# Optimization experiments

Hardware: AMD Instinct MI355X
Metric: run time of the kernel (lower is better)

The kernel has to match this reference:

```python
import jax, jax.numpy as jnp
import numpy as np

B, T, D, H = 4, 1024, 512, 8
DH = D // H
MLP = 4 * D
EPS = 1e-6


def _clinear(xr, xi, Wr, Wi, br, bi):
    # Naive complex Linear = two real nn.Linear layers (each adds its own bias):
    # re = Lr(xr) - Li(xi), im = Lr(xi) + Li(xr)
    re = xr @ Wr.T - xi @ Wi.T + (br - bi)
    im = xi @ Wr.T + xr @ Wi.T + (br + bi)
    return re, im


def _cln(xr, xi):
    # NaiveComplexLayerNorm: real LayerNorm (no affine) on re and im separately
    def ln(v):
        m = jnp.mean(v, -1, keepdims=True)
        va = jnp.var(v, -1, keepdims=True)
        return (v - m) * jax.lax.rsqrt(va + EPS)
    return ln(xr), ln(xi)


def _modulate(xr, xi, shr, shi, scr, sci):
    # complex x * (1 + scale) + shift, scale/shift are [B,D] broadcast over seq
    a, b = (1.0 + scr)[:, None, :], sci[:, None, :]
    return xr * a - xi * b + shr[:, None, :], xr * b + xi * a + shi[:, None, :]


def _gate(gr, gi, xr, xi):
    a, b = gr[:, None, :], gi[:, None, :]
    return xr * a - xi * b, xr * b + xi * a


def _heads(x):  # [B,T,D] -> [B,H,T,DH]
    return x.reshape(B, T, H, DH).transpose(0, 2, 1, 3)


def reference(x_re, x_im, c_re, c_im,
              ada_Wr, ada_Wi, ada_br, ada_bi,
              q_Wr, q_Wi, q_br, q_bi,
              k_Wr, k_Wi, k_br, k_bi,
              v_Wr, v_Wi, v_br, v_bi,
              o_Wr, o_Wi, o_br, o_bi,
              f1_Wr, f1_Wi, f1_br, f1_bi,
              f2_Wr, f2_Wi, f2_br, f2_bi):
    # adaLN_modulation: complex SiLU -> complex Linear -> 6 chunks along dim 1
    sr, si = jax.nn.silu(c_re), jax.nn.silu(c_im)
    mr, mi = _clinear(sr, si, ada_Wr, ada_Wi, ada_br, ada_bi)
    sh_ar, sc_ar, g_ar, sh_mr, sc_mr, g_mr = jnp.split(mr, 6, axis=1)
    sh_ai, sc_ai, g_ai, sh_mi, sc_mi, g_mi = jnp.split(mi, 6, axis=1)

    nr, ni = _cln(x_re, x_im)
    hr, hi = _modulate(nr, ni, sh_ar, sh_ai, sc_ar, sc_ai)

    qr, qi = _clinear(hr, hi, q_Wr, q_Wi, q_br, q_bi)
    kr, ki = _clinear(hr, hi, k_Wr, k_Wi, k_br, k_bi)
    vr, vi = _clinear(hr, hi, v_Wr, v_Wi, v_br, v_bi)
    qr, qi, kr, ki, vr, vi = map(_heads, (qr, qi, kr, ki, vr, vi))

    scale = 1.0 / jnp.sqrt(jnp.float32(DH))
    # complex scores q @ k^T (no conjugation, matching plain complex matmul)
    s_re = (jnp.einsum('bhqd,bhkd->bhqk', qr, kr) - jnp.einsum('bhqd,bhkd->bhqk', qi, ki)) * scale
    s_im = (jnp.einsum('bhqd,bhkd->bhqk', qr, ki) + jnp.einsum('bhqd,bhkd->bhqk', qi, kr)) * scale
    # naive complex softmax: real softmax applied to re/im independently
    a_re = jax.nn.softmax(s_re, axis=-1)
    a_im = jax.nn.softmax(s_im, axis=-1)
    o_r = jnp.einsum('bhqk,bhkd->bhqd', a_re, vr) - jnp.einsum('bhqk,bhkd->bhqd', a_im, vi)
    o_i = jnp.einsum('bhqk,bhkd->bhqd', a_re, vi) + jnp.einsum('bhqk,bhkd->bhqd', a_im, vr)
    o_r = o_r.transpose(0, 2, 1, 3).reshape(B, T, D)
    o_i = o_i.transpose(0, 2, 1, 3).reshape(B, T, D)
    o_r, o_i = _clinear(o_r, o_i, o_Wr, o_Wi, o_br, o_bi)

    gr, gi = _gate(g_ar, g_ai, o_r, o_i)
    x_re, x_im = x_re + gr, x_im + gi

    # ---- MLP branch
    nr, ni = _cln(x_re, x_im)
    hr, hi = _modulate(nr, ni, sh_mr, sh_mi, sc_mr, sc_mi)
    hr, hi = _clinear(hr, hi, f1_Wr, f1_Wi, f1_br, f1_bi)
    hr = jax.nn.gelu(hr, approximate=True)  # ComplexGELU(tanh) per component
    hi = jax.nn.gelu(hi, approximate=True)
    hr, hi = _clinear(hr, hi, f2_Wr, f2_Wi, f2_br, f2_bi)
    gr, gi = _gate(g_mr, g_mi, hr, hi)
    return jnp.stack([x_re + gr, x_im + gi])  # [2,B,T,D] = (real, imag)


def setup_inputs() -> dict:
    key = jax.random.key(0)
    ks = iter(jax.random.split(key, 48))

    def rn(shape, s=1.0):
        return jax.random.normal(next(ks), shape, dtype=jnp.float32) * s

    inp = {'x_re': rn((B, T, D)), 'x_im': rn((B, T, D)),
           'c_re': rn((B, D)), 'c_im': rn((B, D))}

    def lin(name, din, dout):
        inp[name + '_Wr'] = rn((dout, din), 0.02)
        inp[name + '_Wi'] = rn((dout, din), 0.02)
        inp[name + '_br'] = rn((dout,), 0.02)
        inp[name + '_bi'] = rn((dout,), 0.02)

    lin('ada', D, 6 * D)
    for n in ('q', 'k', 'v', 'o'):
        lin(n, D, D)
    lin('f1', D, MLP)
    lin('f2', MLP, D)
    return inp
```

## Files before the change

kernel.cpp:

```cpp
#include <hip/hip_runtime.h>


typedef unsigned short u16;
typedef __attribute__((ext_vector_type(8))) __bf16 bf16x8;
typedef __attribute__((ext_vector_type(8))) u16    u16x8;
typedef __attribute__((ext_vector_type(4))) u16    u16x4;
typedef __attribute__((ext_vector_type(4))) float  f32x4;

#define MFMA16(a, b, c) __builtin_amdgcn_mfma_f32_16x16x32_bf16(a, b, c, 0, 0, 0)

static constexpr int Bd = 4, Td = 1024, Dd = 512, Hd = 8, DHd = 64, MLPd = 2048;

__device__ __forceinline__ u16 f2bf(float x) {
  unsigned int u = __builtin_bit_cast(unsigned int, x);
  u += 0x7fffu + ((u >> 16) & 1u);
  return (u16)(u >> 16);
}
__device__ __forceinline__ bf16x8 ldsfrag(const u16* p) {
  return __builtin_bit_cast(bf16x8, *(const u16x8*)p);
}
__device__ __forceinline__ bf16x8 negbf(bf16x8 v) {
  u16x8 u = __builtin_bit_cast(u16x8, v);
  u ^= (u16)0x8000;
  return __builtin_bit_cast(bf16x8, u);
}
__device__ __forceinline__ float gelu_tanh(float x) {
  float t = tanhf(0.7978845608028654f * (x + 0.044715f * x * x * x));
  return 0.5f * x * (1.f + t);
}

struct CJobs {
  const float* src[12];
  u16* dst[12];
  int blk_start[13];
};
__global__ __launch_bounds__(256) void convert_kernel(CJobs J) {
  const int blk = blockIdx.x;
  int jj = 0;
  while (jj < 11 && blk >= J.blk_start[jj + 1]) ++jj;
  const int idx = (blk - J.blk_start[jj]) * 256 + threadIdx.x;
  const float4 v = ((const float4*)J.src[jj])[idx];
  u16x4 o;
  o[0] = f2bf(v.x); o[1] = f2bf(v.y); o[2] = f2bf(v.z); o[3] = f2bf(v.w);
  *(u16x4*)(J.dst[jj] + (size_t)idx * 4) = o;
}

__global__ __launch_bounds__(256) void ada_kernel(
    const float* __restrict__ c_re, const float* __restrict__ c_im,
    const float* __restrict__ Wr, const float* __restrict__ Wi,
    const float* __restrict__ br, const float* __restrict__ bi,
    float* __restrict__ m_r, float* __restrict__ m_i) {
  __shared__ __align__(16) float sr[512], si[512];
  const int b = blockIdx.x / 12, nb = blockIdx.x % 12;
  const int tid = threadIdx.x;
  for (int i = tid; i < 512; i += 256) {
    const float xr = c_re[b * 512 + i], xi = c_im[b * 512 + i];
    sr[i] = xr / (1.f + __expf(-xr));
    si[i] = xi / (1.f + __expf(-xi));
  }
  __syncthreads();
  const int n = nb * 256 + tid;
  const float4* wr4 = (const float4*)(Wr + (size_t)n * 512);
  const float4* wi4 = (const float4*)(Wi + (size_t)n * 512);
  const float4* sr4 = (const float4*)sr;
  const float4* si4 = (const float4*)si;
  float ar = 0.f, ai = 0.f;
  for (int k = 0; k < 128; ++k) {
    const float4 a_ = sr4[k], b_ = si4[k], u = wr4[k], v = wi4[k];
    ar += a_.x * u.x - b_.x * v.x + a_.y * u.y - b_.y * v.y +
          a_.z * u.z - b_.z * v.z + a_.w * u.w - b_.w * v.w;
    ai += b_.x * u.x + a_.x * v.x + b_.y * u.y + a_.y * v.y +
          b_.z * u.z + a_.z * v.z + b_.w * u.w + a_.w * v.w;
  }
  m_r[(size_t)b * 3072 + n] = ar + br[n] - bi[n];
  m_i[(size_t)b * 3072 + n] = ai + br[n] + bi[n];
}

__global__ __launch_bounds__(256) void ln_mod_kernel(
    const float* __restrict__ xr, const float* __restrict__ xi,
    const float* __restrict__ mv_r, const float* __restrict__ mv_i,
    int off_sh, int off_sc,
    u16* __restrict__ hr, u16* __restrict__ hi) {
  const int row = blockIdx.x;
  const int b = row >> 10;
  const int tid = threadIdx.x;
  const float* xrp = xr + (size_t)row * 512;
  const float* xip = xi + (size_t)row * 512;
  const float r0 = xrp[tid], r1 = xrp[tid + 256];
  const float i0 = xip[tid], i1 = xip[tid + 256];
  float s0 = r0 + r1, s1 = r0 * r0 + r1 * r1;
  float s2 = i0 + i1, s3 = i0 * i0 + i1 * i1;
  #pragma unroll
  for (int o = 32; o > 0; o >>= 1) {
    s0 += __shfl_down(s0, o); s1 += __shfl_down(s1, o);
    s2 += __shfl_down(s2, o); s3 += __shfl_down(s3, o);
  }
  __shared__ float red[4][4];
  if ((tid & 63) == 0) {
    const int wv = tid >> 6;
    red[wv][0] = s0; red[wv][1] = s1; red[wv][2] = s2; red[wv][3] = s3;
  }
  __syncthreads();
  s0 = red[0][0] + red[1][0] + red[2][0] + red[3][0];
  s1 = red[0][1] + red[1][1] + red[2][1] + red[3][1];
  s2 = red[0][2] + red[1][2] + red[2][2] + red[3][2];
  s3 = red[0][3] + red[1][3] + red[2][3] + red[3][3];
  const float mr = s0 * (1.f / 512.f), mi = s2 * (1.f / 512.f);
  const float vr = s1 * (1.f / 512.f) - mr * mr;
  const float vi = s3 * (1.f / 512.f) - mi * mi;
  const float rr = rsqrtf(vr + 1e-6f), ri = rsqrtf(vi + 1e-6f);
  const float* shr = mv_r + (size_t)b * 3072 + off_sh;
  const float* shi = mv_i + (size_t)b * 3072 + off_sh;
  const float* scr = mv_r + (size_t)b * 3072 + off_sc;
  const float* sci = mv_i + (size_t)b * 3072 + off_sc;
  #pragma unroll
  for (int jj = 0; jj < 2; ++jj) {
    const int n = tid + jj * 256;
    const float nr = ((jj ? r1 : r0) - mr) * rr;
    const float ni = ((jj ? i1 : i0) - mi) * ri;
    const float a = 1.f + scr[n], bb = sci[n];
    hr[(size_t)row * 512 + n] = f2bf(nr * a - ni * bb + shr[n]);
    hi[(size_t)row * 512 + n] = f2bf(nr * bb + ni * a + shi[n]);
  }
}

template <int EPI>
__global__ __launch_bounds__(256) void cgemm_kernel(
    const u16* __restrict__ Ar, const u16* __restrict__ Ai,
    const u16* __restrict__ W0r, const u16* __restrict__ W0i,
    const float* __restrict__ b0r, const float* __restrict__ b0i,
    const u16* __restrict__ W1r, const u16* __restrict__ W1i,
    const float* __restrict__ b1r, const float* __restrict__ b1i,
    const u16* __restrict__ W2r, const u16* __restrict__ W2i,
    const float* __restrict__ b2r, const float* __restrict__ b2i,
    int K, int ntiles_per_seg, int out_ld,
    u16* __restrict__ o0r, u16* __restrict__ o0i,
    u16* __restrict__ o1r, u16* __restrict__ o1i,
    u16* __restrict__ o2r, u16* __restrict__ o2i,
    const float* __restrict__ resid_r, const float* __restrict__ resid_i,
    const float* __restrict__ gate_r, const float* __restrict__ gate_i,
    float* __restrict__ ofr, float* __restrict__ ofi) {
  const int seg = blockIdx.y / ntiles_per_seg;
  const int n0 = (blockIdx.y % ntiles_per_seg) * 64;
  const int m0 = blockIdx.x * 64;
  const u16* Wr = (seg == 0) ? W0r : (seg == 1) ? W1r : W2r;
  const u16* Wi = (seg == 0) ? W0i : (seg == 1) ? W1i : W2i;
  const float* br = (seg == 0) ? b0r : (seg == 1) ? b1r : b2r;
  const float* bi = (seg == 0) ? b0i : (seg == 1) ? b1i : b2i;
  u16* obr = (seg == 0) ? o0r : (seg == 1) ? o1r : o2r;
  u16* obi = (seg == 0) ? o0i : (seg == 1) ? o1i : o2i;

  __shared__ __align__(16) u16 sA[2][64 * 72];
  __shared__ __align__(16) u16 sB[2][64 * 72];

  const int tid = threadIdx.x;
  const int w = tid >> 6, lane = tid & 63;
  const int wm = w >> 1, wn = w & 1;
  const int q4 = lane >> 4, c = lane & 15;

  const f32x4 z = {0.f, 0.f, 0.f, 0.f};
  f32x4 accR[2][2], accI[2][2];
  for (int a = 0; a < 2; ++a)
    for (int b2 = 0; b2 < 2; ++b2) { accR[a][b2] = z; accI[a][b2] = z; }

  for (int kt = 0; kt < K; kt += 64) {
    for (int idx = tid; idx < 512; idx += 256) {
      const int row = idx >> 3, cg = idx & 7;
      const int lo = row * 72 + cg * 8;
      *(u16x8*)&sA[0][lo] = *(const u16x8*)(Ar + (size_t)(m0 + row) * K + kt + cg * 8);
      *(u16x8*)&sA[1][lo] = *(const u16x8*)(Ai + (size_t)(m0 + row) * K + kt + cg * 8);
      *(u16x8*)&sB[0][lo] = *(const u16x8*)(Wr + (size_t)(n0 + row) * K + kt + cg * 8);
      *(u16x8*)&sB[1][lo] = *(const u16x8*)(Wi + (size_t)(n0 + row) * K + kt + cg * 8);
    }
    __syncthreads();
    #pragma unroll
    for (int kc = 0; kc < 2; ++kc) {
      bf16x8 a_r[2], a_i[2], a_n[2];
      #pragma unroll
      for (int mi = 0; mi < 2; ++mi) {
        const int off = (wm * 32 + mi * 16 + c) * 72 + kc * 32 + q4 * 8;
        a_r[mi] = ldsfrag(&sA[0][off]);
        a_i[mi] = ldsfrag(&sA[1][off]);
        a_n[mi] = negbf(a_i[mi]);
      }
      #pragma unroll
      for (int ni = 0; ni < 2; ++ni) {
        const int off = (wn * 32 + ni * 16 + c) * 72 + kc * 32 + q4 * 8;
        const bf16x8 b_r = ldsfrag(&sB[0][off]);
        const bf16x8 b_i = ldsfrag(&sB[1][off]);
        #pragma unroll
        for (int mi = 0; mi < 2; ++mi) {
          accR[mi][ni] = MFMA16(a_r[mi], b_r, accR[mi][ni]);
          accR[mi][ni] = MFMA16(a_n[mi], b_i, accR[mi][ni]);
          accI[mi][ni] = MFMA16(a_i[mi], b_r, accI[mi][ni]);
          accI[mi][ni] = MFMA16(a_r[mi], b_i, accI[mi][ni]);
        }
      }
    }
    __syncthreads();
  }

  const float scale = (EPI == 0 && seg == 0) ? 0.125f : 1.f;
  #pragma unroll
  for (int mi = 0; mi < 2; ++mi)
    #pragma unroll
    for (int ni = 0; ni < 2; ++ni) {
      const int n = n0 + wn * 32 + ni * 16 + c;
      const float biasr = br[n] - bi[n];
      const float biasi = br[n] + bi[n];
      #pragma unroll
      for (int r = 0; r < 4; ++r) {
        const int m = m0 + wm * 32 + mi * 16 + q4 * 4 + r;
        const float ore = accR[mi][ni][r] + biasr;
        const float oim = accI[mi][ni][r] + biasi;
        if (EPI == 0) {
          obr[(size_t)m * out_ld + n] = f2bf(ore * scale);
          obi[(size_t)m * out_ld + n] = f2bf(oim * scale);
        } else if (EPI == 2) {
          obr[(size_t)m * out_ld + n] = f2bf(gelu_tanh(ore));
          obi[(size_t)m * out_ld + n] = f2bf(gelu_tanh(oim));
        } else {
          const int bb = m >> 10;
          const float gr = gate_r[(size_t)bb * 3072 + n];
          const float gi = gate_i[(size_t)bb * 3072 + n];
          const size_t o = (size_t)m * 512 + n;
          ofr[o] = resid_r[o] + ore * gr - oim * gi;
          ofi[o] = resid_i[o] + ore * gi + oim * gr;
        }
      }
    }
}

__global__ __launch_bounds__(256) void attn_kernel(
    const u16* __restrict__ Qr, const u16* __restrict__ Qi,
    const u16* __restrict__ Kr, const u16* __restrict__ Ki,
    const u16* __restrict__ Vr, const u16* __restrict__ Vi,
    u16* __restrict__ Or, u16* __restrict__ Oi) {
  __shared__ __align__(16) u16 sQ[2][64 * 72];
  __shared__ __align__(16) u16 sK[2][64 * 72];
  __shared__ __align__(16) u16 sV[2][64 * 72];

  const int tid = threadIdx.x;
  const int w = tid >> 6, lane = tid & 63;
  const int q4 = lane >> 4, c = lane & 15;
  const int bh = blockIdx.y, b = bh >> 3, h = bh & 7;
  const int t0 = blockIdx.x * 64;
  const size_t base = (size_t)b * Td * Dd + h * DHd;

  for (int idx = tid; idx < 512; idx += 256) {
    const int row = idx >> 3, cg = idx & 7;
    const size_t g = base + (size_t)(t0 + row) * Dd + cg * 8;
    const int lo = row * 72 + cg * 8;
    *(u16x8*)&sQ[0][lo] = *(const u16x8*)(Qr + g);
    *(u16x8*)&sQ[1][lo] = *(const u16x8*)(Qi + g);
  }
  __syncthreads();
  bf16x8 aQr[2], aQi[2], aQn[2];
  #pragma unroll
  for (int kc = 0; kc < 2; ++kc) {
    const int off = (w * 16 + c) * 72 + kc * 32 + q4 * 8;
    aQr[kc] = ldsfrag(&sQ[0][off]);
    aQi[kc] = ldsfrag(&sQ[1][off]);
    aQn[kc] = negbf(aQi[kc]);
  }

  float mst[2][4], lst[2][4];
  #pragma unroll
  for (int p = 0; p < 2; ++p)
    for (int r = 0; r < 4; ++r) { mst[p][r] = -1e30f; lst[p][r] = 0.f; }
  const f32x4 z = {0.f, 0.f, 0.f, 0.f};
  f32x4 U1[4], U2[4], U3[4], U4[4];
  for (int i = 0; i < 4; ++i) { U1[i] = z; U2[i] = z; U3[i] = z; U4[i] = z; }

  for (int kt = 0; kt < 16; ++kt) {
    for (int idx = tid; idx < 512; idx += 256) {
      const int row = idx >> 3, cg = idx & 7;
      const size_t g = base + (size_t)(kt * 64 + row) * Dd + cg * 8;
      const int lo = row * 72 + cg * 8;
      *(u16x8*)&sK[0][lo] = *(const u16x8*)(Kr + g);
      *(u16x8*)&sK[1][lo] = *(const u16x8*)(Ki + g);
      const u16x8 vvr = *(const u16x8*)(Vr + g);
      const u16x8 vvi = *(const u16x8*)(Vi + g);
      #pragma unroll
      for (int j = 0; j < 8; ++j) {
        sV[0][(cg * 8 + j) * 72 + row] = vvr[j];
        sV[1][(cg * 8 + j) * 72 + row] = vvi[j];
      }
    }
    __syncthreads();

    f32x4 S[2][4];
    #pragma unroll
    for (int nb = 0; nb < 4; ++nb) {
      f32x4 tr = z, ti = z;
      #pragma unroll
      for (int kc = 0; kc < 2; ++kc) {
        const int off = (nb * 16 + c) * 72 + kc * 32 + q4 * 8;
        const bf16x8 bKr = ldsfrag(&sK[0][off]);
        const bf16x8 bKi = ldsfrag(&sK[1][off]);
        tr = MFMA16(aQr[kc], bKr, tr);
        tr = MFMA16(aQn[kc], bKi, tr);
        ti = MFMA16(aQi[kc], bKr, ti);
        ti = MFMA16(aQr[kc], bKi, ti);
      }
      S[0][nb] = tr; S[1][nb] = ti;
    }
    __syncthreads();

    float alpha[2][4];
    #pragma unroll
    for (int p = 0; p < 2; ++p) {
      float rs[4];
      #pragma unroll
      for (int r = 0; r < 4; ++r) {
        float tm = fmaxf(fmaxf(S[p][0][r], S[p][1][r]), fmaxf(S[p][2][r], S[p][3][r]));
        #pragma unroll
        for (int o = 1; o < 16; o <<= 1) tm = fmaxf(tm, __shfl_xor(tm, o));
        const float mn = fmaxf(mst[p][r], tm);
        alpha[p][r] = __expf(mst[p][r] - mn);
        mst[p][r] = mn;
        rs[r] = 0.f;
      }
      #pragma unroll
      for (int nb = 0; nb < 4; ++nb)
        #pragma unroll
        for (int r = 0; r < 4; ++r) {
          const float pv = __expf(S[p][nb][r] - mst[p][r]);
          rs[r] += pv;
          sK[p][(w * 16 + q4 * 4 + r) * 72 + nb * 16 + c] = f2bf(pv);
        }
      #pragma unroll
      for (int r = 0; r < 4; ++r) {
        float s = rs[r];
        #pragma unroll
        for (int o = 1; o < 16; o <<= 1) s += __shfl_xor(s, o);
        lst[p][r] = lst[p][r] * alpha[p][r] + s;
      }
    }
    #pragma unroll
    for (int i = 0; i < 4; ++i)
      #pragma unroll
      for (int r = 0; r < 4; ++r) {
        U1[i][r] *= alpha[0][r]; U2[i][r] *= alpha[0][r];
        U3[i][r] *= alpha[1][r]; U4[i][r] *= alpha[1][r];
      }
    asm volatile("s_waitcnt lgkmcnt(0)" ::: "memory");
    #pragma unroll
    for (int kc = 0; kc < 2; ++kc) {
      const int poff = (w * 16 + c) * 72 + kc * 32 + q4 * 8;
      const bf16x8 aPr = ldsfrag(&sK[0][poff]);
      const bf16x8 aPi = ldsfrag(&sK[1][poff]);
      #pragma unroll
      for (int nd = 0; nd < 4; ++nd) {
        const int voff = (nd * 16 + c) * 72 + kc * 32 + q4 * 8;
        const bf16x8 bVr = ldsfrag(&sV[0][voff]);
        const bf16x8 bVi = ldsfrag(&sV[1][voff]);
        U1[nd] = MFMA16(aPr, bVr, U1[nd]);
        U2[nd] = MFMA16(aPr, bVi, U2[nd]);
        U3[nd] = MFMA16(aPi, bVr, U3[nd]);
        U4[nd] = MFMA16(aPi, bVi, U4[nd]);
      }
    }
    __syncthreads();
  }

  #pragma unroll
  for (int nd = 0; nd < 4; ++nd)
    #pragma unroll
    for (int r = 0; r < 4; ++r) {
      const int trow = t0 + w * 16 + q4 * 4 + r;
      const int d = nd * 16 + c;
      const float ilre = 1.f / lst[0][r], ilim = 1.f / lst[1][r];
      const float ore = U1[nd][r] * ilre - U4[nd][r] * ilim;
      const float oim = U2[nd][r] * ilre + U3[nd][r] * ilim;
      const size_t g = base + (size_t)trow * Dd + d;
      Or[g] = f2bf(ore);
      Oi[g] = f2bf(oim);
    }
}

extern "C" void kernel_launch(void* const* d_in, const int* in_sizes, int n_in,
                              void* d_out, int out_size, void* d_ws, size_t ws_size,
                              hipStream_t stream) {
  const float* x_re  = (const float*)d_in[0];
  const float* x_im  = (const float*)d_in[1];
  const float* c_re  = (const float*)d_in[2];
  const float* c_im  = (const float*)d_in[3];
  const float* adaWr = (const float*)d_in[4];
  const float* adaWi = (const float*)d_in[5];
  const float* adabr = (const float*)d_in[6];
  const float* adabi = (const float*)d_in[7];
  const float* qWr = (const float*)d_in[8],  *qWi = (const float*)d_in[9];
  const float* qbr = (const float*)d_in[10], *qbi = (const float*)d_in[11];
  const float* kWr = (const float*)d_in[12], *kWi = (const float*)d_in[13];
  const float* kbr = (const float*)d_in[14], *kbi = (const float*)d_in[15];
  const float* vWr = (const float*)d_in[16], *vWi = (const float*)d_in[17];
  const float* vbr = (const float*)d_in[18], *vbi = (const float*)d_in[19];
  const float* oWr = (const float*)d_in[20], *oWi = (const float*)d_in[21];
  const float* obr = (const float*)d_in[22], *obi = (const float*)d_in[23];
  const float* f1Wr = (const float*)d_in[24], *f1Wi = (const float*)d_in[25];
  const float* f1br = (const float*)d_in[26], *f1bi = (const float*)d_in[27];
  const float* f2Wr = (const float*)d_in[28], *f2Wi = (const float*)d_in[29];
  const float* f2br = (const float*)d_in[30], *f2bi = (const float*)d_in[31];

  char* wsp = (char*)d_ws;
  size_t off = 0;
  auto alloc = [&](size_t bytes) -> void* {
    void* p = wsp + off;
    off += (bytes + 255) & ~(size_t)255;
    return p;
  };
  const size_t WQ = 512 * 512, WF = 2048 * 512;
  u16* wqr = (u16*)alloc(WQ * 2); u16* wqi = (u16*)alloc(WQ * 2);
  u16* wkr = (u16*)alloc(WQ * 2); u16* wki = (u16*)alloc(WQ * 2);
  u16* wvr = (u16*)alloc(WQ * 2); u16* wvi = (u16*)alloc(WQ * 2);
  u16* wor = (u16*)alloc(WQ * 2); u16* woi = (u16*)alloc(WQ * 2);
  u16* wf1r = (u16*)alloc(WF * 2); u16* wf1i = (u16*)alloc(WF * 2);
  u16* wf2r = (u16*)alloc(WF * 2); u16* wf2i = (u16*)alloc(WF * 2);
  float* m_r = (float*)alloc(4 * 3072 * 4);
  float* m_i = (float*)alloc(4 * 3072 * 4);
  const size_t ACT = (size_t)Bd * Td * Dd;
  u16* h1r = (u16*)alloc(ACT * 2); u16* h1i = (u16*)alloc(ACT * 2);
  u16* qbr_ = (u16*)alloc(ACT * 2); u16* qbi_ = (u16*)alloc(ACT * 2);
  u16* kbr_ = (u16*)alloc(ACT * 2); u16* kbi_ = (u16*)alloc(ACT * 2);
  u16* vbr_ = (u16*)alloc(ACT * 2); u16* vbi_ = (u16*)alloc(ACT * 2);
  u16* atr = (u16*)alloc(ACT * 2); u16* ati = (u16*)alloc(ACT * 2);
  float* x2r = (float*)alloc(ACT * 4); float* x2i = (float*)alloc(ACT * 4);
  u16* h2r = h1r; u16* h2i = h1i;
  u16* f1or = qbr_;
  u16* f1oi = qbr_ + (size_t)Bd * Td * MLPd;

  CJobs J;
  const float* wsrc[12] = {qWr, qWi, kWr, kWi, vWr, vWi, oWr, oWi, f1Wr, f1Wi, f2Wr, f2Wi};
  u16* wdst[12] = {wqr, wqi, wkr, wki, wvr, wvi, wor, woi, wf1r, wf1i, wf2r, wf2i};
  int cum = 0;
  for (int j = 0; j < 12; ++j) {
    J.src[j] = wsrc[j]; J.dst[j] = wdst[j]; J.blk_start[j] = cum;
    cum += (j < 8 ? (int)WQ : (int)WF) / 1024;
  }
  J.blk_start[12] = cum;
  convert_kernel<<<cum, 256, 0, stream>>>(J);

  ada_kernel<<<48, 256, 0, stream>>>(c_re, c_im, adaWr, adaWi, adabr, adabi, m_r, m_i);

  ln_mod_kernel<<<4096, 256, 0, stream>>>(x_re, x_im, m_r, m_i, 0, 512, h1r, h1i);

  cgemm_kernel<0><<<dim3(64, 24), 256, 0, stream>>>(
      h1r, h1i, wqr, wqi, qbr, qbi, wkr, wki, kbr, kbi, wvr, wvi, vbr, vbi,
      512, 8, 512, qbr_, qbi_, kbr_, kbi_, vbr_, vbi_,
      nullptr, nullptr, nullptr, nullptr, nullptr, nullptr);

  attn_kernel<<<dim3(16, 32), 256, 0, stream>>>(qbr_, qbi_, kbr_, kbi_, vbr_, vbi_, atr, ati);

  cgemm_kernel<1><<<dim3(64, 8), 256, 0, stream>>>(
      atr, ati, wor, woi, obr, obi, wor, woi, obr, obi, wor, woi, obr, obi,
      512, 8, 512, nullptr, nullptr, nullptr, nullptr, nullptr, nullptr,
      x_re, x_im, m_r + 1024, m_i + 1024, x2r, x2i);

  ln_mod_kernel<<<4096, 256, 0, stream>>>(x2r, x2i, m_r, m_i, 1536, 2048, h2r, h2i);

  cgemm_kernel<2><<<dim3(64, 32), 256, 0, stream>>>(
      h2r, h2i, wf1r, wf1i, f1br, f1bi, wf1r, wf1i, f1br, f1bi, wf1r, wf1i, f1br, f1bi,
      512, 32, 2048, f1or, f1oi, nullptr, nullptr, nullptr, nullptr,
      nullptr, nullptr, nullptr, nullptr, nullptr, nullptr);

  float* outp = (float*)d_out;
  cgemm_kernel<3><<<dim3(64, 8), 256, 0, stream>>>(
      f1or, f1oi, wf2r, wf2i, f2br, f2bi, wf2r, wf2i, f2br, f2bi, wf2r, wf2i, f2br, f2bi,
      2048, 8, 512, nullptr, nullptr, nullptr, nullptr, nullptr, nullptr,
      x2r, x2i, m_r + 2560, m_i + 2560, outp, outp + ACT);
}
```

Baseline: 460.9 us.

## Enlarge complex GEMM tiles with direct-to-LDS loads and pre-transpose V

```diff
diff --git a/kernel.cpp b/kernel.cpp
--- a/kernel.cpp
+++ b/kernel.cpp
@@ -2,6 +2,7 @@
 
 
 typedef unsigned short u16;
+typedef unsigned int   u32;
 typedef __attribute__((ext_vector_type(8))) __bf16 bf16x8;
 typedef __attribute__((ext_vector_type(8))) u16    u16x8;
 typedef __attribute__((ext_vector_type(4))) u16    u16x4;
@@ -27,6 +28,11 @@
 __device__ __forceinline__ float gelu_tanh(float x) {
   float t = tanhf(0.7978845608028654f * (x + 0.044715f * x * x * x));
   return 0.5f * x * (1.f + t);
+}
+__device__ __forceinline__ void gload_lds16(const u16* g, u16* l) {
+  __builtin_amdgcn_global_load_lds(
+      (const __attribute__((address_space(1))) u32*)g,
+      (__attribute__((address_space(3))) u32*)l, 16, 0, 0);
 }
 
 struct CJobs {
@@ -124,7 +130,7 @@
   }
 }
 
-template <int EPI>
+template <int TN, int EPI>
 __global__ __launch_bounds__(256) void cgemm_kernel(
     const u16* __restrict__ Ar, const u16* __restrict__ Ai,
     const u16* __restrict__ W0r, const u16* __restrict__ W0i,
@@ -140,9 +146,12 @@
     const float* __restrict__ resid_r, const float* __restrict__ resid_i,
     const float* __restrict__ gate_r, const float* __restrict__ gate_i,
     float* __restrict__ ofr, float* __restrict__ ofi) {
+  constexpr int NI = TN / 32;
+  constexpr int PB = TN / 16;
+  constexpr int NSTAGE = 16 + 2 * PB;
   const int seg = blockIdx.y / ntiles_per_seg;
-  const int n0 = (blockIdx.y % ntiles_per_seg) * 64;
-  const int m0 = blockIdx.x * 64;
+  const int n0 = (blockIdx.y % ntiles_per_seg) * TN;
+  const int m0 = blockIdx.x * 128;
   const u16* Wr = (seg == 0) ? W0r : (seg == 1) ? W1r : W2r;
   const u16* Wi = (seg == 0) ? W0i : (seg == 1) ? W1i : W2i;
   const float* br = (seg == 0) ? b0r : (seg == 1) ? b1r : b2r;
@@ -150,67 +159,84 @@
   u16* obr = (seg == 0) ? o0r : (seg == 1) ? o1r : o2r;
   u16* obi = (seg == 0) ? o0i : (seg == 1) ? o1i : o2i;
 
-  __shared__ __align__(16) u16 sA[2][64 * 72];
-  __shared__ __align__(16) u16 sB[2][64 * 72];
+  __shared__ __align__(16) u16 sAr[128 * 32], sAi[128 * 32];
+  __shared__ __align__(16) u16 sBr[TN * 32], sBi[TN * 32];
 
   const int tid = threadIdx.x;
   const int w = tid >> 6, lane = tid & 63;
   const int wm = w >> 1, wn = w & 1;
   const int q4 = lane >> 4, c = lane & 15;
+  const int r16 = lane >> 2, cseg = (lane & 3) * 8;
+
+  auto stage = [&](int kt) {
+    #pragma unroll
+    for (int I = w; I < NSTAGE; I += 4) {
+      const u16* src; u16* dst;
+      if (I < 16) {
+        const int p = I >> 3, sub = I & 7;
+        src = (p ? Ai : Ar) + (size_t)(m0 + sub * 16 + r16) * K + kt + cseg;
+        dst = (p ? sAi : sAr) + sub * 512;
+      } else {
+        const int J = I - 16;
+        const int p = J / PB, sub = J % PB;
+        src = (p ? Wi : Wr) + (size_t)(n0 + sub * 16 + r16) * K + kt + cseg;
+        dst = (p ? sBi : sBr) + sub * 512;
+      }
+      gload_lds16(src, dst);
+    }
+  };
 
   const f32x4 z = {0.f, 0.f, 0.f, 0.f};
-  f32x4 accR[2][2], accI[2][2];
-  for (int a = 0; a < 2; ++a)
-    for (int b2 = 0; b2 < 2; ++b2) { accR[a][b2] = z; accI[a][b2] = z; }
-
-  for (int kt = 0; kt < K; kt += 64) {
-    for (int idx = tid; idx < 512; idx += 256) {
-      const int row = idx >> 3, cg = idx & 7;
-      const int lo = row * 72 + cg * 8;
-      *(u16x8*)&sA[0][lo] = *(const u16x8*)(Ar + (size_t)(m0 + row) * K + kt + cg * 8);
-      *(u16x8*)&sA[1][lo] = *(const u16x8*)(Ai + (size_t)(m0 + row) * K + kt + cg * 8);
-      *(u16x8*)&sB[0][lo] = *(const u16x8*)(Wr + (size_t)(n0 + row) * K + kt + cg * 8);
-      *(u16x8*)&sB[1][lo] = *(const u16x8*)(Wi + (size_t)(n0 + row) * K + kt + cg * 8);
+  f32x4 accR[4][NI], accI[4][NI];
+  #pragma unroll
+  for (int a = 0; a < 4; ++a)
+    #pragma unroll
+    for (int b2 = 0; b2 < NI; ++b2) { accR[a][b2] = z; accI[a][b2] = z; }
+
+  stage(0);
+  asm volatile("s_waitcnt vmcnt(0)" ::: "memory");
+  __syncthreads();
+  for (int kt = 0; kt < K; kt += 32) {
+    bf16x8 a_r[4], a_i[4], a_n[4];
+    #pragma unroll
+    for (int mi = 0; mi < 4; ++mi) {
+      const int off = (wm * 64 + mi * 16 + c) * 32 + q4 * 8;
+      a_r[mi] = ldsfrag(sAr + off);
+      a_i[mi] = ldsfrag(sAi + off);
+      a_n[mi] = negbf(a_i[mi]);
+    }
+    #pragma unroll
+    for (int ni = 0; ni < NI; ++ni) {
+      const int off = (wn * (TN / 2) + ni * 16 + c) * 32 + q4 * 8;
+      const bf16x8 b_r = ldsfrag(sBr + off);
+      const bf16x8 b_i = ldsfrag(sBi + off);
+      #pragma unroll
+      for (int mi = 0; mi < 4; ++mi) {
+        accR[mi][ni] = MFMA16(a_r[mi], b_r, accR[mi][ni]);
+        accR[mi][ni] = MFMA16(a_n[mi], b_i, accR[mi][ni]);
+        accI[mi][ni] = MFMA16(a_i[mi], b_r, accI[mi][ni]);
+        accI[mi][ni] = MFMA16(a_r[mi], b_i, accI[mi][ni]);
+      }
     }
     __syncthreads();
-    #pragma unroll
-    for (int kc = 0; kc < 2; ++kc) {
-      bf16x8 a_r[2], a_i[2], a_n[2];
-      #pragma unroll
-      for (int mi = 0; mi < 2; ++mi) {
-        const int off = (wm * 32 + mi * 16 + c) * 72 + kc * 32 + q4 * 8;
-        a_r[mi] = ldsfrag(&sA[0][off]);
-        a_i[mi] = ldsfrag(&sA[1][off]);
-        a_n[mi] = negbf(a_i[mi]);
-      }
-      #pragma unroll
-      for (int ni = 0; ni < 2; ++ni) {
-        const int off = (wn * 32 + ni * 16 + c) * 72 + kc * 32 + q4 * 8;
-        const bf16x8 b_r = ldsfrag(&sB[0][off]);
-        const bf16x8 b_i = ldsfrag(&sB[1][off]);
-        #pragma unroll
-        for (int mi = 0; mi < 2; ++mi) {
-          accR[mi][ni] = MFMA16(a_r[mi], b_r, accR[mi][ni]);
-          accR[mi][ni] = MFMA16(a_n[mi], b_i, accR[mi][ni]);
-          accI[mi][ni] = MFMA16(a_i[mi], b_r, accI[mi][ni]);
-          accI[mi][ni] = MFMA16(a_r[mi], b_i, accI[mi][ni]);
-        }
-      }
-    }
-    __syncthreads();
+    if (kt + 32 < K) {
+      stage(kt + 32);
+      asm volatile("s_waitcnt vmcnt(0)" ::: "memory");
+      __syncthreads();
+    }
   }
 
   const float scale = (EPI == 0 && seg == 0) ? 0.125f : 1.f;
   #pragma unroll
-  for (int mi = 0; mi < 2; ++mi)
-    #pragma unroll
-    for (int ni = 0; ni < 2; ++ni) {
-      const int n = n0 + wn * 32 + ni * 16 + c;
+  for (int mi = 0; mi < 4; ++mi)
+    #pragma unroll
+    for (int ni = 0; ni < NI; ++ni) {
+      const int n = n0 + wn * (TN / 2) + ni * 16 + c;
       const float biasr = br[n] - bi[n];
       const float biasi = br[n] + bi[n];
       #pragma unroll
       for (int r = 0; r < 4; ++r) {
-        const int m = m0 + wm * 32 + mi * 16 + q4 * 4 + r;
+        const int m = m0 + wm * 64 + mi * 16 + q4 * 4 + r;
         const float ore = accR[mi][ni][r] + biasr;
         const float oim = accI[mi][ni][r] + biasi;
         if (EPI == 0) {
@@ -231,14 +257,44 @@
     }
 }
 
+__global__ __launch_bounds__(256) void vt_kernel(
+    const u16* __restrict__ Vr, const u16* __restrict__ Vi,
+    u16* __restrict__ vTr, u16* __restrict__ vTi) {
+  __shared__ __align__(16) u16 tile[2][64 * 64];
+  const int tid = threadIdx.x;
+  const int tt = blockIdx.x, bh = blockIdx.y, b = bh >> 3, h = bh & 7;
+  const size_t base = (size_t)b * Td * Dd + h * DHd;
+  for (int idx = tid; idx < 512; idx += 256) {
+    const int t = idx >> 3, dblk = idx & 7;
+    const size_t g = base + (size_t)(tt * 64 + t) * Dd + dblk * 8;
+    const int o = t * 64 + ((dblk ^ (t >> 3)) << 3);
+    *(u16x8*)&tile[0][o] = *(const u16x8*)(Vr + g);
+    *(u16x8*)&tile[1][o] = *(const u16x8*)(Vi + g);
+  }
+  __syncthreads();
+  for (int idx = tid; idx < 512; idx += 256) {
+    const int d = idx >> 3, cg = idx & 7;
+    u16x8 o0, o1;
+    #pragma unroll
+    for (int j = 0; j < 8; ++j) {
+      const int t = cg * 8 + j;
+      const int o = t * 64 + (((d >> 3) ^ (t >> 3)) << 3) + (d & 7);
+      o0[j] = tile[0][o];
+      o1[j] = tile[1][o];
+    }
+    const size_t g = ((size_t)bh * 64 + d) * Td + tt * 64 + cg * 8;
+    *(u16x8*)(vTr + g) = o0;
+    *(u16x8*)(vTi + g) = o1;
+  }
+}
+
 __global__ __launch_bounds__(256) void attn_kernel(
     const u16* __restrict__ Qr, const u16* __restrict__ Qi,
     const u16* __restrict__ Kr, const u16* __restrict__ Ki,
-    const u16* __restrict__ Vr, const u16* __restrict__ Vi,
+    const u16* __restrict__ vTr, const u16* __restrict__ vTi,
     u16* __restrict__ Or, u16* __restrict__ Oi) {
-  __shared__ __align__(16) u16 sQ[2][64 * 72];
+  __shared__ __align__(16) u16 sQV[2][64 * 72];
   __shared__ __align__(16) u16 sK[2][64 * 72];
-  __shared__ __align__(16) u16 sV[2][64 * 72];
 
   const int tid = threadIdx.x;
   const int w = tid >> 6, lane = tid & 63;
@@ -246,23 +302,25 @@
   const int bh = blockIdx.y, b = bh >> 3, h = bh & 7;
   const int t0 = blockIdx.x * 64;
   const size_t base = (size_t)b * Td * Dd + h * DHd;
+  const size_t vbase = (size_t)bh * 64 * Td;
 
   for (int idx = tid; idx < 512; idx += 256) {
     const int row = idx >> 3, cg = idx & 7;
     const size_t g = base + (size_t)(t0 + row) * Dd + cg * 8;
     const int lo = row * 72 + cg * 8;
-    *(u16x8*)&sQ[0][lo] = *(const u16x8*)(Qr + g);
-    *(u16x8*)&sQ[1][lo] = *(const u16x8*)(Qi + g);
+    *(u16x8*)&sQV[0][lo] = *(const u16x8*)(Qr + g);
+    *(u16x8*)&sQV[1][lo] = *(const u16x8*)(Qi + g);
   }
   __syncthreads();
   bf16x8 aQr[2], aQi[2], aQn[2];
   #pragma unroll
   for (int kc = 0; kc < 2; ++kc) {
     const int off = (w * 16 + c) * 72 + kc * 32 + q4 * 8;
-    aQr[kc] = ldsfrag(&sQ[0][off]);
-    aQi[kc] = ldsfrag(&sQ[1][off]);
+    aQr[kc] = ldsfrag(&sQV[0][off]);
+    aQi[kc] = ldsfrag(&sQV[1][off]);
     aQn[kc] = negbf(aQi[kc]);
   }
+  __syncthreads();
 
   float mst[2][4], lst[2][4];
   #pragma unroll
@@ -275,17 +333,13 @@
   for (int kt = 0; kt < 16; ++kt) {
     for (int idx = tid; idx < 512; idx += 256) {
       const int row = idx >> 3, cg = idx & 7;
-      const size_t g = base + (size_t)(kt * 64 + row) * Dd + cg * 8;
       const int lo = row * 72 + cg * 8;
-      *(u16x8*)&sK[0][lo] = *(const u16x8*)(Kr + g);
-      *(u16x8*)&sK[1][lo] = *(const u16x8*)(Ki + g);
-      const u16x8 vvr = *(const u16x8*)(Vr + g);
-      const u16x8 vvi = *(const u16x8*)(Vi + g);
-      #pragma unroll
-      for (int j = 0; j < 8; ++j) {
-        sV[0][(cg * 8 + j) * 72 + row] = vvr[j];
-        sV[1][(cg * 8 + j) * 72 + row] = vvi[j];
-      }
+      const size_t gk = base + (size_t)(kt * 64 + row) * Dd + cg * 8;
+      *(u16x8*)&sK[0][lo] = *(const u16x8*)(Kr + gk);
+      *(u16x8*)&sK[1][lo] = *(const u16x8*)(Ki + gk);
+      const size_t gv = vbase + (size_t)row * Td + kt * 64 + cg * 8;
+      *(u16x8*)&sQV[0][lo] = *(const u16x8*)(vTr + gv);
+      *(u16x8*)&sQV[1][lo] = *(const u16x8*)(vTi + gv);
     }
     __syncthreads();
 
@@ -353,8 +407,8 @@
       #pragma unroll
       for (int nd = 0; nd < 4; ++nd) {
         const int voff = (nd * 16 + c) * 72 + kc * 32 + q4 * 8;
-        const bf16x8 bVr = ldsfrag(&sV[0][voff]);
-        const bf16x8 bVi = ldsfrag(&sV[1][voff]);
+        const bf16x8 bVr = ldsfrag(&sQV[0][voff]);
+        const bf16x8 bVi = ldsfrag(&sQV[1][voff]);
         U1[nd] = MFMA16(aPr, bVr, U1[nd]);
         U2[nd] = MFMA16(aPr, bVi, U2[nd]);
         U3[nd] = MFMA16(aPi, bVr, U3[nd]);
@@ -426,6 +480,7 @@
   u16* vbr_ = (u16*)alloc(ACT * 2); u16* vbi_ = (u16*)alloc(ACT * 2);
   u16* atr = (u16*)alloc(ACT * 2); u16* ati = (u16*)alloc(ACT * 2);
   float* x2r = (float*)alloc(ACT * 4); float* x2i = (float*)alloc(ACT * 4);
+  u16* vtr = (u16*)alloc(ACT * 2); u16* vti = (u16*)alloc(ACT * 2);
   u16* h2r = h1r; u16* h2i = h1i;
   u16* f1or = qbr_;
   u16* f1oi = qbr_ + (size_t)Bd * Td * MLPd;
@@ -445,27 +500,29 @@
 
   ln_mod_kernel<<<4096, 256, 0, stream>>>(x_re, x_im, m_r, m_i, 0, 512, h1r, h1i);
 
-  cgemm_kernel<0><<<dim3(64, 24), 256, 0, stream>>>(
+  cgemm_kernel<128, 0><<<dim3(32, 12), 256, 0, stream>>>(
       h1r, h1i, wqr, wqi, qbr, qbi, wkr, wki, kbr, kbi, wvr, wvi, vbr, vbi,
-      512, 8, 512, qbr_, qbi_, kbr_, kbi_, vbr_, vbi_,
+      512, 4, 512, qbr_, qbi_, kbr_, kbi_, vbr_, vbi_,
       nullptr, nullptr, nullptr, nullptr, nullptr, nullptr);
 
-  attn_kernel<<<dim3(16, 32), 256, 0, stream>>>(qbr_, qbi_, kbr_, kbi_, vbr_, vbi_, atr, ati);
-
-  cgemm_kernel<1><<<dim3(64, 8), 256, 0, stream>>>(
+  vt_kernel<<<dim3(16, 32), 256, 0, stream>>>(vbr_, vbi_, vtr, vti);
+
+  attn_kernel<<<dim3(16, 32), 256, 0, stream>>>(qbr_, qbi_, kbr_, kbi_, vtr, vti, atr, ati);
+
+  cgemm_kernel<64, 1><<<dim3(32, 8), 256, 0, stream>>>(
       atr, ati, wor, woi, obr, obi, wor, woi, obr, obi, wor, woi, obr, obi,
       512, 8, 512, nullptr, nullptr, nullptr, nullptr, nullptr, nullptr,
       x_re, x_im, m_r + 1024, m_i + 1024, x2r, x2i);
 
   ln_mod_kernel<<<4096, 256, 0, stream>>>(x2r, x2i, m_r, m_i, 1536, 2048, h2r, h2i);
 
-  cgemm_kernel<2><<<dim3(64, 32), 256, 0, stream>>>(
+  cgemm_kernel<128, 2><<<dim3(32, 16), 256, 0, stream>>>(
       h2r, h2i, wf1r, wf1i, f1br, f1bi, wf1r, wf1i, f1br, f1bi, wf1r, wf1i, f1br, f1bi,
-      512, 32, 2048, f1or, f1oi, nullptr, nullptr, nullptr, nullptr,
+      512, 16, 2048, f1or, f1oi, nullptr, nullptr, nullptr, nullptr,
       nullptr, nullptr, nullptr, nullptr, nullptr, nullptr);
 
   float* outp = (float*)d_out;
-  cgemm_kernel<3><<<dim3(64, 8), 256, 0, stream>>>(
+  cgemm_kernel<64, 3><<<dim3(32, 8), 256, 0, stream>>>(
       f1or, f1oi, wf2r, wf2i, f2br, f2bi, wf2r, wf2i, f2br, f2bi, wf2r, wf2i, f2br, f2bi,
       2048, 8, 512, nullptr, nullptr, nullptr, nullptr, nullptr, nullptr,
       x2r, x2i, m_r + 2560, m_i + 2560, outp, outp + ACT);
```

New measurement: 747.1 us. 1.62x slower.
